# Kernel tuning notes

Hardware: AMD Instinct MI355X
Metric: run time of the kernel (lower is better)

Reference implementation:

```python
import jax, jax.numpy as jnp
import numpy as np
from jax import lax

N = 4096
B = 16
DT_STEP = 0.1   # integration step dt
NT = 500        # number of timesteps; T = NT * dt = 50
TAUSYN = 8.0
# EIF neuron defaults from the module
TAUM, EL, VTH, VRE, VT_, DT_EIF, VLB = 10.0, -72.0, 0.0, -72.0, -55.0, 1.0, -85.0


def setup_inputs() -> dict:
    key = jax.random.key(0)
    k1, k2, k3 = jax.random.split(key, 3)
    W = jax.random.normal(k1, (N, N), dtype=jnp.float32) / np.sqrt(N).astype(np.float32)
    x0 = jax.random.normal(k2, (B, N), dtype=jnp.float32)
    # initial_V='random': uniform in [Vre, VT)
    V0 = VRE + (VT_ - VRE) * jax.random.uniform(k3, (B, N), dtype=jnp.float32)
    Y0 = jnp.zeros((B, N), dtype=jnp.float32)
    return {"W": W, "x0": x0, "V0": V0, "Y0": Y0}


def reference(W, x0, V0, Y0):
    dt = DT_STEP
    T = NT * dt
    inv_dt = 1.0 / dt

    def step(carry, _):
        V, Y, r = carry
        # recurrent_layer(Y) + x0  (nn.Linear applies W: Y @ W^T)
        Z = jnp.matmul(Y, W.T) + x0
        # EIF membrane dynamics, Euler step, lower-bound clamp
        dV = (-(V - EL) + DT_EIF * jnp.exp((V - VT_) / DT_EIF) + Z) / TAUM
        V = jnp.maximum(V + dt * dV, VLB)
        spike = V >= VTH
        S = jnp.where(spike, inv_dt, 0.0).astype(V.dtype)
        V = jnp.where(spike, VRE, V)
        # synaptic trace decay
        Y = Y + (dt / TAUSYN) * (-Y + S)
        return (V, Y, r + S), None

    r0 = jnp.zeros_like(x0)
    (V, Y, r), _ = lax.scan(step, (V0, Y0, r0), None, length=NT)
    # Tburn = 0: r *= dt / (T - Tburn)
    return r * (dt / T)
```

## Files before the change

kernel.cpp:

```cpp
#include <hip/hip_runtime.h>
#include <math.h>


#define NN 4096


__global__ __launch_bounds__(256) void spec_kernel(const float* __restrict__ W,
                                                   const float* __restrict__ x0,
                                                   const float* __restrict__ V0,
                                                   const float* __restrict__ Y0,
                                                   float* __restrict__ zrec,
                                                   int* __restrict__ sflags,
                                                   float* __restrict__ out) {
    __shared__ float yrow[NN];
    __shared__ unsigned long long m[4];
    const int t = threadIdx.x;
    const int gid = blockIdx.x * 256 + t;
    const int b = blockIdx.x >> 4;
    const int n = gid & (NN - 1);

    const int4* Yr4 = (const int4*)(Y0 + (size_t)b * NN);
    int4 o = {0, 0, 0, 0};
#pragma unroll
    for (int i = 0; i < 4; ++i) {
        int4 q = Yr4[i * 256 + t];
        o.x |= q.x; o.y |= q.y; o.z |= q.z; o.w |= q.w;
    }
    int ynz = __syncthreads_or(o.x | o.y | o.z | o.w);

    float z0 = 0.0f;
    if (ynz) {
        const float4* Yr = (const float4*)(Y0 + (size_t)b * NN);
#pragma unroll
        for (int i = 0; i < 4; ++i)
            ((float4*)yrow)[i * 256 + t] = Yr[i * 256 + t];
        __syncthreads();
        const float4* Wr = (const float4*)(W + (size_t)n * NN);
        float4 a = {0.0f, 0.0f, 0.0f, 0.0f};
        for (int k = 0; k < NN / 4; ++k) {
            float4 y = ((const float4*)yrow)[k];
            float4 w = Wr[k];
            a.x = fmaf(y.x, w.x, a.x);
            a.y = fmaf(y.y, w.y, a.y);
            a.z = fmaf(y.z, w.z, a.z);
            a.w = fmaf(y.w, w.w, a.w);
        }
        z0 = (a.x + a.y) + (a.z + a.w);
    }
    zrec[gid] = z0;

    float v = V0[gid];
    const float c = fmaf(0.01f, x0[gid], -0.72f);
    float vmax = v, vmin = v;
    const float L2E = 1.44269504088896f;
    const float K55 = 55.0f * 1.44269504088896f;

    if (z0 == 0.0f) {
#pragma unroll 10
        for (int s = 0; s < 500; ++s) {
            float e = __builtin_amdgcn_exp2f(fmaf(v, L2E, K55));
            float w = fmaf(0.99f, v, c);
            v = fmaf(0.01f, e, w);
            vmax = fmaxf(vmax, v);
            vmin = fminf(vmin, v);
        }
    } else {
        float z = z0 * 0.01f;
        float czt = c + z;
#pragma unroll 10
        for (int s = 0; s < 500; ++s) {
            float e = __builtin_amdgcn_exp2f(fmaf(v, L2E, K55));
            float w = fmaf(0.99f, v, czt);
            v = fmaf(0.01f, e, w);
            vmax = fmaxf(vmax, v);
            vmin = fminf(vmin, v);
            z *= 0.9875f;
            czt = c + z;
        }
    }

    bool fb = (vmax >= 0.0f) || !(vmin >= -85.0f);
    unsigned long long bal = __ballot(fb);
    if ((t & 63) == 0) m[t >> 6] = bal;
    __syncthreads();
    if (t == 0) sflags[blockIdx.x] = (m[0] | m[1] | m[2] | m[3]) ? 1 : 0;

    out[gid] = 0.0f;
}


__global__ __launch_bounds__(1024) void persist_kernel(const float* __restrict__ W,
                                                       const float* __restrict__ x0,
                                                       const float* __restrict__ V0,
                                                       const int* __restrict__ sflags,
                                                       float* __restrict__ zrec,
                                                       float* __restrict__ out) {
    const int t = threadIdx.x;
    const int lane = t & 63;

    bool spk = false;
#pragma unroll
    for (int i = 0; i < 4; ++i) spk |= (sflags[lane + 64 * i] != 0);
    if (!__any(spk)) return;

    __shared__ unsigned long long masks[2][16];
    __shared__ int cnt;
    __shared__ int list[4096];

    const int b = blockIdx.x;
    const int wv = t >> 6;
    const int n0 = t * 4;
    const size_t base = (size_t)b * NN + n0;

    float4 zr = *(const float4*)(zrec + base);
    float4 v  = *(const float4*)(V0 + base);
    float4 xx = *(const float4*)(x0 + base);
    float4 r  = {0.0f, 0.0f, 0.0f, 0.0f};

#pragma unroll 1
    for (int step = 0; step < 500; ++step) {
        const int p = step & 1;

        float z0 = zr.x + xx.x, z1 = zr.y + xx.y, z2 = zr.z + xx.z, z3 = zr.w + xx.w;

        float e0 = expf(v.x + 55.0f), e1 = expf(v.y + 55.0f);
        float e2 = expf(v.z + 55.0f), e3 = expf(v.w + 55.0f);
        v.x = fmaxf(fmaf(0.01f, -(v.x + 72.0f) + e0 + z0, v.x), -85.0f);
        v.y = fmaxf(fmaf(0.01f, -(v.y + 72.0f) + e1 + z1, v.y), -85.0f);
        v.z = fmaxf(fmaf(0.01f, -(v.z + 72.0f) + e2 + z2, v.z), -85.0f);
        v.w = fmaxf(fmaf(0.01f, -(v.w + 72.0f) + e3 + z3, v.w), -85.0f);

        bool s0 = v.x >= 0.0f, s1 = v.y >= 0.0f, s2 = v.z >= 0.0f, s3 = v.w >= 0.0f;
        if (s0) { v.x = -72.0f; r.x += 10.0f; }
        if (s1) { v.y = -72.0f; r.y += 10.0f; }
        if (s2) { v.z = -72.0f; r.z += 10.0f; }
        if (s3) { v.w = -72.0f; r.w += 10.0f; }

        zr.x *= 0.9875f; zr.y *= 0.9875f; zr.z *= 0.9875f; zr.w *= 0.9875f;

        bool any = s0 | s1 | s2 | s3;
        unsigned long long bal = __ballot(any);
        if (lane == 0) masks[p][wv] = bal;
        __syncthreads();

        unsigned long long tot = 0;
#pragma unroll
        for (int i = 0; i < 16; ++i) tot |= masks[p][i];

        if (tot != 0) {
            if (t == 0) cnt = 0;
            __syncthreads();
            int k = (int)s0 + (int)s1 + (int)s2 + (int)s3;
            if (k) {
                int pos = atomicAdd(&cnt, k);
                if (s0) list[pos++] = n0 + 0;
                if (s1) list[pos++] = n0 + 1;
                if (s2) list[pos++] = n0 + 2;
                if (s3) list[pos++] = n0 + 3;
            }
            __syncthreads();
            int mcnt = cnt;
            for (int s = 0; s < mcnt; ++s) {
                int j = list[s];
                zr.x += 0.125f * W[(size_t)(n0 + 0) * NN + j];
                zr.y += 0.125f * W[(size_t)(n0 + 1) * NN + j];
                zr.z += 0.125f * W[(size_t)(n0 + 2) * NN + j];
                zr.w += 0.125f * W[(size_t)(n0 + 3) * NN + j];
            }
        }
    }

    float4 o = {r.x * 0.002f, r.y * 0.002f, r.z * 0.002f, r.w * 0.002f};
    *(float4*)(out + base) = o;
}

extern "C" void kernel_launch(void* const* d_in, const int* in_sizes, int n_in,
                              void* d_out, int out_size, void* d_ws, size_t ws_size,
                              hipStream_t stream) {
    const float* W  = (const float*)d_in[0];
    const float* x0 = (const float*)d_in[1];
    const float* V0 = (const float*)d_in[2];
    const float* Y0 = (const float*)d_in[3];
    float* out  = (float*)d_out;
    float* ws   = (float*)d_ws;

    float* zrec = ws;
    int* sflags = (int*)(ws + 65536);

    spec_kernel<<<256, 256, 0, stream>>>(W, x0, V0, Y0, zrec, sflags, out);
    persist_kernel<<<16, 1024, 0, stream>>>(W, x0, V0, sflags, zrec, out);
}
```

Measured before the change: 98.72 us.

## Fuse into one kernel and skip simulation via analytic no-spike bound

Two kernels are replaced by one. The old first kernel simulated all 500 steps per neuron just to prove that no spikes occur. The new kernel uses an analytic invariant instead: with zero initial trace, V ≤ -55 and x0 ≤ 8 keep the membrane below threshold forever. When that holds for every neuron in a batch row, the block writes zeros and exits. Otherwise it computes the recurrent input in-block and runs the existing event-driven persistent loop, which removes the workspace round-trip and the second launch, at the cost of fewer, larger blocks for the matvec fallback.

Result: faster. 90.57 us (-8.3%).

```diff
diff --git a/kernel.cpp b/kernel.cpp
--- a/kernel.cpp
+++ b/kernel.cpp
@@ -4,118 +4,64 @@
 
 #define NN 4096
 
+__global__ __launch_bounds__(1024) void fused_kernel(const float* __restrict__ W,
+                                                     const float* __restrict__ x0,
+                                                     const float* __restrict__ V0,
+                                                     const float* __restrict__ Y0,
+                                                     float* __restrict__ out) {
+    __shared__ float yrow[NN];
+    __shared__ unsigned long long masks[2][16];
+    __shared__ int cnt;
+    __shared__ int list[NN];
 
-__global__ __launch_bounds__(256) void spec_kernel(const float* __restrict__ W,
-                                                   const float* __restrict__ x0,
-                                                   const float* __restrict__ V0,
-                                                   const float* __restrict__ Y0,
-                                                   float* __restrict__ zrec,
-                                                   int* __restrict__ sflags,
-                                                   float* __restrict__ out) {
-    __shared__ float yrow[NN];
-    __shared__ unsigned long long m[4];
     const int t = threadIdx.x;
-    const int gid = blockIdx.x * 256 + t;
-    const int b = blockIdx.x >> 4;
-    const int n = gid & (NN - 1);
+    const int lane = t & 63;
+    const int wv = t >> 6;
+    const int b = blockIdx.x;
+    const int n0 = t * 4;
+    const size_t base = (size_t)b * NN + n0;
 
-    const int4* Yr4 = (const int4*)(Y0 + (size_t)b * NN);
-    int4 o = {0, 0, 0, 0};
-#pragma unroll
-    for (int i = 0; i < 4; ++i) {
-        int4 q = Yr4[i * 256 + t];
-        o.x |= q.x; o.y |= q.y; o.z |= q.z; o.w |= q.w;
-    }
-    int ynz = __syncthreads_or(o.x | o.y | o.z | o.w);
+    float4 v  = *(const float4*)(V0 + base);
+    float4 xx = *(const float4*)(x0 + base);
+    int4  yq  = *(const int4*)(Y0 + base);
 
-    float z0 = 0.0f;
-    if (ynz) {
-        const float4* Yr = (const float4*)(Y0 + (size_t)b * NN);
-#pragma unroll
-        for (int i = 0; i < 4; ++i)
-            ((float4*)yrow)[i * 256 + t] = Yr[i * 256 + t];
-        __syncthreads();
-        const float4* Wr = (const float4*)(W + (size_t)n * NN);
-        float4 a = {0.0f, 0.0f, 0.0f, 0.0f};
-        for (int k = 0; k < NN / 4; ++k) {
-            float4 y = ((const float4*)yrow)[k];
-            float4 w = Wr[k];
-            a.x = fmaf(y.x, w.x, a.x);
-            a.y = fmaf(y.y, w.y, a.y);
-            a.z = fmaf(y.z, w.z, a.z);
-            a.w = fmaf(y.w, w.w, a.w);
-        }
-        z0 = (a.x + a.y) + (a.z + a.w);
-    }
-    zrec[gid] = z0;
+    const int ynz = __syncthreads_or(yq.x | yq.y | yq.z | yq.w);
 
-    float v = V0[gid];
-    const float c = fmaf(0.01f, x0[gid], -0.72f);
-    float vmax = v, vmin = v;
-    const float L2E = 1.44269504088896f;
-    const float K55 = 55.0f * 1.44269504088896f;
-
-    if (z0 == 0.0f) {
-#pragma unroll 10
-        for (int s = 0; s < 500; ++s) {
-            float e = __builtin_amdgcn_exp2f(fmaf(v, L2E, K55));
-            float w = fmaf(0.99f, v, c);
-            v = fmaf(0.01f, e, w);
-            vmax = fmaxf(vmax, v);
-            vmin = fminf(vmin, v);
-        }
-    } else {
-        float z = z0 * 0.01f;
-        float czt = c + z;
-#pragma unroll 10
-        for (int s = 0; s < 500; ++s) {
-            float e = __builtin_amdgcn_exp2f(fmaf(v, L2E, K55));
-            float w = fmaf(0.99f, v, czt);
-            v = fmaf(0.01f, e, w);
-            vmax = fmaxf(vmax, v);
-            vmin = fminf(vmin, v);
-            z *= 0.9875f;
-            czt = c + z;
+    if (!ynz) {
+        const bool ok = (v.x <= -55.0f) && (v.y <= -55.0f) &&
+                        (v.z <= -55.0f) && (v.w <= -55.0f) &&
+                        (xx.x <= 8.0f) && (xx.y <= 8.0f) &&
+                        (xx.z <= 8.0f) && (xx.w <= 8.0f);
+        if (__syncthreads_and((int)ok)) {
+            float4 zero = {0.0f, 0.0f, 0.0f, 0.0f};
+            *(float4*)(out + base) = zero;
+            return;
         }
     }
 
-    bool fb = (vmax >= 0.0f) || !(vmin >= -85.0f);
-    unsigned long long bal = __ballot(fb);
-    if ((t & 63) == 0) m[t >> 6] = bal;
-    __syncthreads();
-    if (t == 0) sflags[blockIdx.x] = (m[0] | m[1] | m[2] | m[3]) ? 1 : 0;
+    float4 zr = {0.0f, 0.0f, 0.0f, 0.0f};
+    if (ynz) {
+        ((float4*)yrow)[t] = *(const float4*)&yq;
+        __syncthreads();
+        const float* W0 = W + (size_t)(n0 + 0) * NN;
+        const float* W1 = W + (size_t)(n0 + 1) * NN;
+        const float* W2 = W + (size_t)(n0 + 2) * NN;
+        const float* W3 = W + (size_t)(n0 + 3) * NN;
+        for (int j = 0; j < NN; j += 4) {
+            float4 y  = ((const float4*)yrow)[j >> 2];
+            float4 w0 = *(const float4*)(W0 + j);
+            float4 w1 = *(const float4*)(W1 + j);
+            float4 w2 = *(const float4*)(W2 + j);
+            float4 w3 = *(const float4*)(W3 + j);
+            zr.x = fmaf(y.x, w0.x, fmaf(y.y, w0.y, fmaf(y.z, w0.z, fmaf(y.w, w0.w, zr.x))));
+            zr.y = fmaf(y.x, w1.x, fmaf(y.y, w1.y, fmaf(y.z, w1.z, fmaf(y.w, w1.w, zr.y))));
+            zr.z = fmaf(y.x, w2.x, fmaf(y.y, w2.y, fmaf(y.z, w2.z, fmaf(y.w, w2.w, zr.z))));
+            zr.w = fmaf(y.x, w3.x, fmaf(y.y, w3.y, fmaf(y.z, w3.z, fmaf(y.w, w3.w, zr.w))));
+        }
+        __syncthreads();
+    }
 
-    out[gid] = 0.0f;
-}
-
-
-__global__ __launch_bounds__(1024) void persist_kernel(const float* __restrict__ W,
-                                                       const float* __restrict__ x0,
-                                                       const float* __restrict__ V0,
-                                                       const int* __restrict__ sflags,
-                                                       float* __restrict__ zrec,
-                                                       float* __restrict__ out) {
-    const int t = threadIdx.x;
-    const int lane = t & 63;
-
-    bool spk = false;
-#pragma unroll
-    for (int i = 0; i < 4; ++i) spk |= (sflags[lane + 64 * i] != 0);
-    if (!__any(spk)) return;
-
-    __shared__ unsigned long long masks[2][16];
-    __shared__ int cnt;
-    __shared__ int list[4096];
-
-    const int b = blockIdx.x;
-    const int wv = t >> 6;
-    const int n0 = t * 4;
-    const size_t base = (size_t)b * NN + n0;
-
-    float4 zr = *(const float4*)(zrec + base);
-    float4 v  = *(const float4*)(V0 + base);
-    float4 xx = *(const float4*)(x0 + base);
-    float4 r  = {0.0f, 0.0f, 0.0f, 0.0f};
+    float4 r = {0.0f, 0.0f, 0.0f, 0.0f};
 
 #pragma unroll 1
     for (int step = 0; step < 500; ++step) {
@@ -181,12 +127,8 @@
     const float* x0 = (const float*)d_in[1];
     const float* V0 = (const float*)d_in[2];
     const float* Y0 = (const float*)d_in[3];
-    float* out  = (float*)d_out;
-    float* ws   = (float*)d_ws;
+    float* out = (float*)d_out;
+    (void)d_ws; (void)ws_size;
 
-    float* zrec = ws;
-    int* sflags = (int*)(ws + 65536);
-
-    spec_kernel<<<256, 256, 0, stream>>>(W, x0, V0, Y0, zrec, sflags, out);
-    persist_kernel<<<16, 1024, 0, stream>>>(W, x0, V0, sflags, zrec, out);
+    fused_kernel<<<16, 1024, 0, stream>>>(W, x0, V0, Y0, out);
 }
```
